# Kernel optimization log

Measured on AMD Instinct MI355X. Metric: run time of the kernel, lower is better.

The kernel has to match this reference:

```python
import jax, jax.numpy as jnp
import numpy as np

N, H, D = 4096, 8, 256  # num_nodes, num_heads, in==out channels
E = 131072
SLOPE = 0.2
NEG_INF = -1.0e9


def setup_inputs() -> dict:
    key = jax.random.key(0)
    k1, k2, k3, k4, k5, k6 = jax.random.split(key, 6)
    x = jax.random.normal(k1, (N, D), dtype=jnp.float32)
    edge_index = jax.random.randint(k2, (2, E), 0, N, dtype=jnp.int64)
    linear_weight = jax.random.normal(k3, (H, D, D), dtype=jnp.float32)
    query_weight = jax.random.normal(k4, (H, 1, D), dtype=jnp.float32)
    key_weight = jax.random.normal(k5, (H, 1, D), dtype=jnp.float32)
    return {
        "x": x,
        "linear_weight": linear_weight,
        "query_weight": query_weight,
        "key_weight": key_weight,
        "edge_index": edge_index,
    }


def reference(x, linear_weight, query_weight, key_weight, edge_index):
    n = x.shape[0]
    # lt[h,i,n] = sum_k W[h,i,k] * x[n,k]   (torch: matmul(W, x^T)) -> [H, D, N]
    lt = jnp.einsum('hik,nk->hin', linear_weight, x)
    # q,k: [H,1,D] @ [H,D,N] -> [H,1,N]
    q = jnp.einsum('hod,hdn->hon', query_weight, lt)
    k = jnp.einsum('hod,hdn->hon', key_weight, lt)
    # torch: matmul(q [H,1,N], k^T [H,N,1]) -> [H,1,1] scalar per head
    att = jnp.einsum('hon,hon->h', q, k)[:, None, None]
    att = jax.nn.leaky_relu(att, SLOPE)
    # dense adjacency (to_dense_adj sums duplicate edges)
    adj = jnp.zeros((n, n), dtype=x.dtype).at[edge_index[0], edge_index[1]].add(1.0)
    # broadcast scalar att over [H,N,N], mask non-edges
    masked = jnp.where(adj[None, :, :] == 0, jnp.asarray(NEG_INF, x.dtype), att)
    attn = jax.nn.softmax(masked, axis=2)  # [H,N,N]
    value = jnp.swapaxes(lt, 1, 2)  # [H,N,D]
    out = jnp.einsum('hnm,hmd->hnd', attn, value)  # [H,N,D]
    return jnp.transpose(out, (1, 0, 2)).reshape(n, -1)  # [N, H*D]
```

## Files before the change

### kernel.cpp

```cpp
#include <hip/hip_runtime.h>
#include <hip/hip_bf16.h>


constexpr int NN = 4096;
constexpr int DD = 256;
constexpr int EE = 131072;
constexpr int MW = NN / 32;
constexpr int NOUT = 2048;
constexpr int LCAP = 256;

constexpr size_t OFF_COLSUM = (size_t)NN * MW * 4;
constexpr size_t OFF_AGGB   = OFF_COLSUM + DD * 4;
constexpr size_t OFF_LWB    = OFF_AGGB + (size_t)NN * DD * 2;
constexpr int ZERO_F4 = (int)(OFF_AGGB / 16);

typedef __attribute__((ext_vector_type(4))) float f32x4;
typedef __attribute__((ext_vector_type(8))) short s16x8;

__device__ inline short f2bf(float f) {
    __hip_bfloat16 h = __float2bfloat16(f);
    return *reinterpret_cast<short*>(&h);
}

__global__ __launch_bounds__(256) void init_k(const float* __restrict__ w,
                                              short* __restrict__ wb,
                                              float4* __restrict__ zbase) {
    int b = blockIdx.x, t = threadIdx.x;
    if (b < 513) {
        int idx = b * 256 + t;
        if (idx < ZERO_F4) zbase[idx] = make_float4(0.f, 0.f, 0.f, 0.f);
    } else {
        int i = (b - 513) * 256 + t;
        float4 v = reinterpret_cast<const float4*>(w)[i];
        short4 o;
        o.x = f2bf(v.x); o.y = f2bf(v.y); o.z = f2bf(v.z); o.w = f2bf(v.w);
        reinterpret_cast<short4*>(wb)[i] = o;
    }
}

__global__ __launch_bounds__(256) void edges_k(
        const int* __restrict__ ei, int stride, unsigned int* __restrict__ mask,
        const float* __restrict__ x, float* __restrict__ colsum) {
    int b = blockIdx.x, t = threadIdx.x;
    if (b < 512) {
        int e = b * 256 + t;
        int u = ei[(size_t)e * stride];
        int v = ei[((size_t)EE + e) * stride];
        atomicOr(&mask[(size_t)u * MW + (v >> 5)], 1u << (v & 31));
    } else {
        int r0 = (b - 512) * 64;
        float acc = 0.f;
        for (int r = 0; r < 64; ++r) acc += x[(size_t)(r0 + r) * DD + t];
        atomicAdd(&colsum[t], acc);
    }
}

__global__ __launch_bounds__(256) void agg_k(
        const float* __restrict__ x, const unsigned int* __restrict__ mask,
        const float* __restrict__ colsum, short* __restrict__ aggb) {
    __shared__ int nbr[4][LCAP];
    __shared__ int cnt[4];
    const int t = threadIdx.x;
    const int r = t >> 6;
    const int lane = t & 63;
    const int row = blockIdx.x * 4 + r;

    if (lane == 0) cnt[r] = 0;
    __syncthreads();
    const unsigned int* mr = &mask[(size_t)row * MW];
#pragma unroll
    for (int j = 0; j < 2; ++j) {
        unsigned int m = mr[lane * 2 + j];
        while (m) {
            int b = __ffs(m) - 1;
            m &= m - 1;
            int idx = atomicAdd(&cnt[r], 1);
            if (idx < LCAP) nbr[r][idx] = (lane * 2 + j) * 32 + b;
        }
    }
    __syncthreads();
    const int deg = min(cnt[r], LCAP);
    const int c4 = lane << 2;

    float4 acc = make_float4(0.f, 0.f, 0.f, 0.f);
    for (int q0 = 0; q0 < deg; q0 += 4) {
        int nn[4];
        float4 v[4];
#pragma unroll
        for (int j = 0; j < 4; ++j)
            nn[j] = nbr[r][(q0 + j < deg) ? q0 + j : q0];
#pragma unroll
        for (int j = 0; j < 4; ++j)
            v[j] = *reinterpret_cast<const float4*>(&x[(size_t)nn[j] * DD + c4]);
#pragma unroll
        for (int j = 0; j < 4; ++j)
            if (q0 + j < deg) {
                acc.x += v[j].x; acc.y += v[j].y;
                acc.z += v[j].z; acc.w += v[j].w;
            }
    }
    float4 res;
    if (deg > 0) {
        float inv = 1.f / (float)deg;
        res = make_float4(acc.x * inv, acc.y * inv, acc.z * inv, acc.w * inv);
    } else {
        float4 cs = *reinterpret_cast<const float4*>(&colsum[c4]);
        float inv = 1.f / (float)NN;
        res = make_float4(cs.x * inv, cs.y * inv, cs.z * inv, cs.w * inv);
    }
    short4 o;
    o.x = f2bf(res.x); o.y = f2bf(res.y); o.z = f2bf(res.z); o.w = f2bf(res.w);
    *reinterpret_cast<short4*>(&aggb[(size_t)row * DD + c4]) = o;
}

constexpr int BK = 32;
constexpr int PADK = 40;

__global__ __launch_bounds__(256, 2) void gemm_k(
        const short* __restrict__ A, const short* __restrict__ B,
        float* __restrict__ C) {
    __shared__ short As[2][128][PADK];
    __shared__ short Bs[2][128][PADK];
    const int t = threadIdx.x;
    const int lane = t & 63;
    const int wv = t >> 6;
    const int wr = wv >> 1, wc = wv & 1;
    const int m0 = blockIdx.y * 128;
    const int n0 = blockIdx.x * 128;
    const int lr = lane & 15;
    const int lk = (lane >> 4) * 8;
    const int srow = t >> 2;
    const int skc = (t & 3) * 8;

    f32x4 acc[4][4] = {};
    s16x8 ra0, ra1, rb0, rb1;

#define LOADG(k0)                                                           \
    {                                                                       \
        ra0 = *reinterpret_cast<const s16x8*>(&A[(size_t)(m0 + srow) * DD + (k0) + skc]);      \
        ra1 = *reinterpret_cast<const s16x8*>(&A[(size_t)(m0 + 64 + srow) * DD + (k0) + skc]); \
        rb0 = *reinterpret_cast<const s16x8*>(&B[(size_t)(n0 + srow) * DD + (k0) + skc]);      \
        rb1 = *reinterpret_cast<const s16x8*>(&B[(size_t)(n0 + 64 + srow) * DD + (k0) + skc]); \
    }
#define WRITEL(buf)                                                         \
    {                                                                       \
        *reinterpret_cast<s16x8*>(&As[buf][srow][skc]) = ra0;               \
        *reinterpret_cast<s16x8*>(&As[buf][srow + 64][skc]) = ra1;          \
        *reinterpret_cast<s16x8*>(&Bs[buf][srow][skc]) = rb0;               \
        *reinterpret_cast<s16x8*>(&Bs[buf][srow + 64][skc]) = rb1;          \
    }

    LOADG(0)
    WRITEL(0)
    __syncthreads();
    LOADG(BK)

#pragma unroll
    for (int k = 0; k < 8; ++k) {
        const int cur = k & 1;
        if (k < 7) WRITEL(cur ^ 1)
        s16x8 a[4], b[4];
#pragma unroll
        for (int i = 0; i < 4; ++i)
            a[i] = *reinterpret_cast<const s16x8*>(&As[cur][wr * 64 + i * 16 + lr][lk]);
#pragma unroll
        for (int j = 0; j < 4; ++j)
            b[j] = *reinterpret_cast<const s16x8*>(&Bs[cur][wc * 64 + j * 16 + lr][lk]);
        if (k < 6) LOADG((k + 2) * BK)
#pragma unroll
        for (int i = 0; i < 4; ++i)
#pragma unroll
            for (int j = 0; j < 4; ++j)
                acc[i][j] = __builtin_amdgcn_mfma_f32_16x16x32_bf16(
                    a[i], b[j], acc[i][j], 0, 0, 0);
        __syncthreads();
    }
#undef LOADG
#undef WRITEL

    const int crow = (lane >> 4) * 4;
    const int ccol = lane & 15;
#pragma unroll
    for (int i = 0; i < 4; ++i)
#pragma unroll
        for (int j = 0; j < 4; ++j)
#pragma unroll
            for (int r = 0; r < 4; ++r)
                C[(size_t)(m0 + wr * 64 + i * 16 + crow + r) * NOUT
                  + n0 + wc * 64 + j * 16 + ccol] = acc[i][j][r];
}

extern "C" void kernel_launch(void* const* d_in, const int* in_sizes, int n_in,
                              void* d_out, int out_size, void* d_ws, size_t ws_size,
                              hipStream_t stream) {
    const float* x  = (const float*)d_in[0];
    const float* lw = (const float*)d_in[1];
    const int*   ei = (const int*)d_in[4];
    float* out = (float*)d_out;

    char* ws = (char*)d_ws;
    unsigned int* mask   = (unsigned int*)ws;
    float*        colsum = (float*)(ws + OFF_COLSUM);
    short*        aggb   = (short*)(ws + OFF_AGGB);
    short*        lwb    = (short*)(ws + OFF_LWB);

    int stride = (in_sizes[4] == 2 * EE) ? 1 : 2;

    init_k<<<513 + 512, 256, 0, stream>>>(lw, lwb, (float4*)ws);
    edges_k<<<512 + 64, 256, 0, stream>>>(ei, stride, mask, x, colsum);
    agg_k<<<NN / 4, 256, 0, stream>>>(x, mask, colsum, aggb);

    dim3 ggrid(NOUT / 128, NN / 128);
    gemm_k<<<ggrid, 256, 0, stream>>>(aggb, lwb, out);
}
```

Baseline: 40.94 us.

## Fuse edge scan and aggregation per row block; convert weights inside GEMM

Replaces the init, edge-mask, colsum and aggregation kernels with one kernel. Each block of 16 rows scans the whole edge list and builds its adjacency bitmask in shared memory, which removes the global mask zeroing, global atomics and the separate weight conversion kernel. The GEMM now loads fp32 weights and converts them to bf16 while staging them into LDS. The trade-off is that every one of the 256 blocks reads all 131072 edge sources, a redundant read. It also drops the int64 stride detection, assumes 32-bit indices, and lowers the per-row neighbour cap to 128.

New measurement: 100.9 us. 2.46x slower.

```diff
diff --git a/kernel.cpp b/kernel.cpp
--- a/kernel.cpp
+++ b/kernel.cpp
@@ -7,12 +7,11 @@
 constexpr int EE = 131072;
 constexpr int MW = NN / 32;
 constexpr int NOUT = 2048;
-constexpr int LCAP = 256;
-
-constexpr size_t OFF_COLSUM = (size_t)NN * MW * 4;
-constexpr size_t OFF_AGGB   = OFF_COLSUM + DD * 4;
-constexpr size_t OFF_LWB    = OFF_AGGB + (size_t)NN * DD * 2;
-constexpr int ZERO_F4 = (int)(OFF_AGGB / 16);
+constexpr int RPB = 16;
+constexpr int NBA = NN / RPB;
+constexpr int LCAP = 128;
+constexpr int BK = 32;
+constexpr int PADK = 40;
 
 typedef __attribute__((ext_vector_type(4))) float f32x4;
 typedef __attribute__((ext_vector_type(8))) short s16x8;
@@ -21,103 +20,95 @@
     __hip_bfloat16 h = __float2bfloat16(f);
     return *reinterpret_cast<short*>(&h);
 }
-
-__global__ __launch_bounds__(256) void init_k(const float* __restrict__ w,
-                                              short* __restrict__ wb,
-                                              float4* __restrict__ zbase) {
-    int b = blockIdx.x, t = threadIdx.x;
-    if (b < 513) {
-        int idx = b * 256 + t;
-        if (idx < ZERO_F4) zbase[idx] = make_float4(0.f, 0.f, 0.f, 0.f);
-    } else {
-        int i = (b - 513) * 256 + t;
-        float4 v = reinterpret_cast<const float4*>(w)[i];
+__device__ inline s16x8 cvt8(const float4& a, const float4& b) {
+    s16x8 o;
+    o[0] = f2bf(a.x); o[1] = f2bf(a.y); o[2] = f2bf(a.z); o[3] = f2bf(a.w);
+    o[4] = f2bf(b.x); o[5] = f2bf(b.y); o[6] = f2bf(b.z); o[7] = f2bf(b.w);
+    return o;
+}
+
+__global__ __launch_bounds__(512) void scan_agg_k(
+        const float* __restrict__ x, const int* __restrict__ eu,
+        const int* __restrict__ ev, short* __restrict__ aggb) {
+    __shared__ unsigned int bm[RPB][MW];
+    __shared__ int nbr[RPB][LCAP];
+    __shared__ int cnt[RPB];
+    const int t = threadIdx.x;
+    const int row0 = blockIdx.x * RPB;
+
+    for (int i = t; i < RPB * MW; i += 512) ((unsigned int*)bm)[i] = 0u;
+    if (t < RPB) cnt[t] = 0;
+    __syncthreads();
+
+    for (int e = t; e < EE; e += 512) {
+        int u = eu[e];
+        if ((unsigned)(u - row0) < (unsigned)RPB) {
+            int v = ev[e];
+            atomicOr(&bm[u - row0][v >> 5], 1u << (v & 31));
+        }
+    }
+    __syncthreads();
+
+    const int wv = t >> 6;
+    const int lane = t & 63;
+#pragma unroll
+    for (int rr = 0; rr < 2; ++rr) {
+        const int r = wv * 2 + rr;
+#pragma unroll
+        for (int j = 0; j < 2; ++j) {
+            unsigned int m = bm[r][lane * 2 + j];
+            while (m) {
+                int b = __ffs(m) - 1;
+                m &= m - 1;
+                int idx = atomicAdd(&cnt[r], 1);
+                if (idx < LCAP) nbr[r][idx] = (lane * 2 + j) * 32 + b;
+            }
+        }
+    }
+    __syncthreads();
+
+    const int c4 = lane << 2;
+#pragma unroll
+    for (int rr = 0; rr < 2; ++rr) {
+        const int r = wv * 2 + rr;
+        const int deg = min(cnt[r], LCAP);
+        float4 acc = make_float4(0.f, 0.f, 0.f, 0.f);
+        for (int q0 = 0; q0 < deg; q0 += 8) {
+            int nn[8];
+            float4 v[8];
+#pragma unroll
+            for (int j = 0; j < 8; ++j)
+                nn[j] = nbr[r][(q0 + j < deg) ? q0 + j : q0];
+#pragma unroll
+            for (int j = 0; j < 8; ++j)
+                v[j] = *reinterpret_cast<const float4*>(&x[(size_t)nn[j] * DD + c4]);
+#pragma unroll
+            for (int j = 0; j < 8; ++j)
+                if (q0 + j < deg) {
+                    acc.x += v[j].x; acc.y += v[j].y;
+                    acc.z += v[j].z; acc.w += v[j].w;
+                }
+        }
+        float inv;
+        if (deg > 0) {
+            inv = 1.f / (float)deg;
+        } else {
+            acc = make_float4(0.f, 0.f, 0.f, 0.f);
+            for (int n = 0; n < NN; ++n) {
+                float4 v = *reinterpret_cast<const float4*>(&x[(size_t)n * DD + c4]);
+                acc.x += v.x; acc.y += v.y; acc.z += v.z; acc.w += v.w;
+            }
+            inv = 1.f / (float)NN;
+        }
         short4 o;
-        o.x = f2bf(v.x); o.y = f2bf(v.y); o.z = f2bf(v.z); o.w = f2bf(v.w);
-        reinterpret_cast<short4*>(wb)[i] = o;
-    }
-}
-
-__global__ __launch_bounds__(256) void edges_k(
-        const int* __restrict__ ei, int stride, unsigned int* __restrict__ mask,
-        const float* __restrict__ x, float* __restrict__ colsum) {
-    int b = blockIdx.x, t = threadIdx.x;
-    if (b < 512) {
-        int e = b * 256 + t;
-        int u = ei[(size_t)e * stride];
-        int v = ei[((size_t)EE + e) * stride];
-        atomicOr(&mask[(size_t)u * MW + (v >> 5)], 1u << (v & 31));
-    } else {
-        int r0 = (b - 512) * 64;
-        float acc = 0.f;
-        for (int r = 0; r < 64; ++r) acc += x[(size_t)(r0 + r) * DD + t];
-        atomicAdd(&colsum[t], acc);
-    }
-}
-
-__global__ __launch_bounds__(256) void agg_k(
-        const float* __restrict__ x, const unsigned int* __restrict__ mask,
-        const float* __restrict__ colsum, short* __restrict__ aggb) {
-    __shared__ int nbr[4][LCAP];
-    __shared__ int cnt[4];
-    const int t = threadIdx.x;
-    const int r = t >> 6;
-    const int lane = t & 63;
-    const int row = blockIdx.x * 4 + r;
-
-    if (lane == 0) cnt[r] = 0;
-    __syncthreads();
-    const unsigned int* mr = &mask[(size_t)row * MW];
-#pragma unroll
-    for (int j = 0; j < 2; ++j) {
-        unsigned int m = mr[lane * 2 + j];
-        while (m) {
-            int b = __ffs(m) - 1;
-            m &= m - 1;
-            int idx = atomicAdd(&cnt[r], 1);
-            if (idx < LCAP) nbr[r][idx] = (lane * 2 + j) * 32 + b;
-        }
-    }
-    __syncthreads();
-    const int deg = min(cnt[r], LCAP);
-    const int c4 = lane << 2;
-
-    float4 acc = make_float4(0.f, 0.f, 0.f, 0.f);
-    for (int q0 = 0; q0 < deg; q0 += 4) {
-        int nn[4];
-        float4 v[4];
-#pragma unroll
-        for (int j = 0; j < 4; ++j)
-            nn[j] = nbr[r][(q0 + j < deg) ? q0 + j : q0];
-#pragma unroll
-        for (int j = 0; j < 4; ++j)
-            v[j] = *reinterpret_cast<const float4*>(&x[(size_t)nn[j] * DD + c4]);
-#pragma unroll
-        for (int j = 0; j < 4; ++j)
-            if (q0 + j < deg) {
-                acc.x += v[j].x; acc.y += v[j].y;
-                acc.z += v[j].z; acc.w += v[j].w;
-            }
-    }
-    float4 res;
-    if (deg > 0) {
-        float inv = 1.f / (float)deg;
-        res = make_float4(acc.x * inv, acc.y * inv, acc.z * inv, acc.w * inv);
-    } else {
-        float4 cs = *reinterpret_cast<const float4*>(&colsum[c4]);
-        float inv = 1.f / (float)NN;
-        res = make_float4(cs.x * inv, cs.y * inv, cs.z * inv, cs.w * inv);
-    }
-    short4 o;
-    o.x = f2bf(res.x); o.y = f2bf(res.y); o.z = f2bf(res.z); o.w = f2bf(res.w);
-    *reinterpret_cast<short4*>(&aggb[(size_t)row * DD + c4]) = o;
-}
-
-constexpr int BK = 32;
-constexpr int PADK = 40;
+        o.x = f2bf(acc.x * inv); o.y = f2bf(acc.y * inv);
+        o.z = f2bf(acc.z * inv); o.w = f2bf(acc.w * inv);
+        *reinterpret_cast<short4*>(&aggb[(size_t)(row0 + r) * DD + c4]) = o;
+    }
+}
 
 __global__ __launch_bounds__(256, 2) void gemm_k(
-        const short* __restrict__ A, const short* __restrict__ B,
+        const short* __restrict__ A, const float* __restrict__ Bf,
         float* __restrict__ C) {
     __shared__ short As[2][128][PADK];
     __shared__ short Bs[2][128][PADK];
@@ -133,21 +124,24 @@
     const int skc = (t & 3) * 8;
 
     f32x4 acc[4][4] = {};
-    s16x8 ra0, ra1, rb0, rb1;
-
-#define LOADG(k0)                                                           \
-    {                                                                       \
-        ra0 = *reinterpret_cast<const s16x8*>(&A[(size_t)(m0 + srow) * DD + (k0) + skc]);      \
-        ra1 = *reinterpret_cast<const s16x8*>(&A[(size_t)(m0 + 64 + srow) * DD + (k0) + skc]); \
-        rb0 = *reinterpret_cast<const s16x8*>(&B[(size_t)(n0 + srow) * DD + (k0) + skc]);      \
-        rb1 = *reinterpret_cast<const s16x8*>(&B[(size_t)(n0 + 64 + srow) * DD + (k0) + skc]); \
+    s16x8 ra0, ra1;
+    float4 rb00, rb01, rb10, rb11;
+
+#define LOADG(k0)                                                                        \
+    {                                                                                    \
+        ra0 = *reinterpret_cast<const s16x8*>(&A[(size_t)(m0 + srow) * DD + (k0) + skc]);       \
+        ra1 = *reinterpret_cast<const s16x8*>(&A[(size_t)(m0 + 64 + srow) * DD + (k0) + skc]);  \
+        rb00 = *reinterpret_cast<const float4*>(&Bf[(size_t)(n0 + srow) * DD + (k0) + skc]);    \
+        rb01 = *reinterpret_cast<const float4*>(&Bf[(size_t)(n0 + srow) * DD + (k0) + skc + 4]);\
+        rb10 = *reinterpret_cast<const float4*>(&Bf[(size_t)(n0 + 64 + srow) * DD + (k0) + skc]);    \
+        rb11 = *reinterpret_cast<const float4*>(&Bf[(size_t)(n0 + 64 + srow) * DD + (k0) + skc + 4]);\
     }
 #define WRITEL(buf)                                                         \
     {                                                                       \
         *reinterpret_cast<s16x8*>(&As[buf][srow][skc]) = ra0;               \
         *reinterpret_cast<s16x8*>(&As[buf][srow + 64][skc]) = ra1;          \
-        *reinterpret_cast<s16x8*>(&Bs[buf][srow][skc]) = rb0;               \
-        *reinterpret_cast<s16x8*>(&Bs[buf][srow + 64][skc]) = rb1;          \
+        *reinterpret_cast<s16x8*>(&Bs[buf][srow][skc]) = cvt8(rb00, rb01);  \
+        *reinterpret_cast<s16x8*>(&Bs[buf][srow + 64][skc]) = cvt8(rb10, rb11); \
     }
 
     LOADG(0)
@@ -198,18 +192,10 @@
     const int*   ei = (const int*)d_in[4];
     float* out = (float*)d_out;
 
-    char* ws = (char*)d_ws;
-    unsigned int* mask   = (unsigned int*)ws;
-    float*        colsum = (float*)(ws + OFF_COLSUM);
-    short*        aggb   = (short*)(ws + OFF_AGGB);
-    short*        lwb    = (short*)(ws + OFF_LWB);
-
-    int stride = (in_sizes[4] == 2 * EE) ? 1 : 2;
-
-    init_k<<<513 + 512, 256, 0, stream>>>(lw, lwb, (float4*)ws);
-    edges_k<<<512 + 64, 256, 0, stream>>>(ei, stride, mask, x, colsum);
-    agg_k<<<NN / 4, 256, 0, stream>>>(x, mask, colsum, aggb);
+    short* aggb = (short*)d_ws;
+
+    scan_agg_k<<<NBA, 512, 0, stream>>>(x, ei, ei + EE, aggb);
 
     dim3 ggrid(NOUT / 128, NN / 128);
-    gemm_k<<<ggrid, 256, 0, stream>>>(aggb, lwb, out);
-}
+    gemm_k<<<ggrid, 256, 0, stream>>>(aggb, lw, out);
+}
```
